# Optimization experiments

Hardware: AMD Instinct MI355X
Metric: run time of the kernel (lower is better)

The kernel has to match this reference:

```python
import jax, jax.numpy as jnp
import numpy as np

D_MODEL = 1024

def setup_inputs() -> dict:
    key = jax.random.key(0)
    ks = jax.random.split(key, 5)
    s = 1.0 / np.sqrt(D_MODEL)  # torch Linear default init scale-ish
    x = jax.random.normal(ks[0], (4, 2048, D_MODEL), dtype=jnp.float32)
    Wq = jax.random.normal(ks[1], (D_MODEL, D_MODEL), dtype=jnp.float32) * s
    Wk = jax.random.normal(ks[2], (D_MODEL, D_MODEL), dtype=jnp.float32) * s
    Wv = jax.random.normal(ks[3], (D_MODEL, D_MODEL), dtype=jnp.float32) * s
    Wo = jax.random.normal(ks[4], (D_MODEL, D_MODEL), dtype=jnp.float32) * s
    z = jnp.zeros((D_MODEL,), dtype=jnp.float32)
    return {"x": x, "Wq": Wq, "bq": z, "Wk": Wk, "bk": z, "Wv": Wv, "bv": z, "Wo": Wo, "bo": z}

def reference(x, Wq, bq, Wk, bk, Wv, bv, Wo, bo):
    # x: (B, S, D). Single-head causal attention, dropout in eval mode (identity).
    B, S, D = x.shape
    Q = jnp.einsum('bsd,ed->bse', x, Wq) + bq
    K = jnp.einsum('bsd,ed->bse', x, Wk) + bk
    V = jnp.einsum('bsd,ed->bse', x, Wv) + bv
    scores = jnp.einsum('bqd,bkd->bqk', Q, K) / jnp.sqrt(jnp.float32(D))
    causal = jnp.tril(jnp.ones((S, S), dtype=bool))  # (S, S)
    scores = jnp.where(causal, scores, -jnp.inf)
    weights = jax.nn.softmax(scores, axis=-1)
    attended = jnp.einsum('bqk,bkd->bqd', weights, V)
    out = jnp.einsum('bsd,ed->bse', attended, Wo) + bo
    return out
```

## Files before the change

### kernel.cpp

```cpp
#include <hip/hip_runtime.h>
#include <cstdint>
#include <cstddef>


#define D_MODEL 1024
#define SEQ     2048
#define BATCH   4

typedef unsigned short u16;
typedef __bf16 bf16_t;
typedef bf16_t bf16x8 __attribute__((ext_vector_type(8)));
typedef float  f32x4  __attribute__((ext_vector_type(4)));
typedef u16    u16x4  __attribute__((ext_vector_type(4)));

__device__ __forceinline__ u16 f2bf(float x) {
  union { float f; uint32_t u; } v; v.f = x;
  uint32_t r = v.u + 0x7fffu + ((v.u >> 16) & 1u);
  return (u16)(r >> 16);
}

__device__ __forceinline__ void gload_lds16(const u16* g, u16* l) {
  __builtin_amdgcn_global_load_lds((__attribute__((address_space(1))) void*)g,
                                   (__attribute__((address_space(3))) void*)l,
                                   16, 0, 0);
}

template <bool ROWSUM>
__device__ __forceinline__ void gemm_core(const u16* __restrict__ Ablk,
                                          const u16* __restrict__ Bblk,
                                          int lda, int ldb, int ksteps64,
                                          u16* As, u16* Bs,
                                          f32x4 acc[4][4], f32x4* rs) {
  const int tid  = threadIdx.x;
  const int wave = tid >> 6, lane = tid & 63;
  const int wr = (wave >> 1) * 64, wc = (wave & 1) * 64;
  const int frow = lane & 15, kq = lane >> 4;
  int sm[4], sk[4];
#pragma unroll
  for (int t = 0; t < 4; ++t) {
    const int ch = t * 256 + tid;
    sm[t] = ch >> 3;
    sk[t] = ((ch & 7) ^ (sm[t] & 7)) * 8;
  }
  int aoff[4], boff[4];
#pragma unroll
  for (int i = 0; i < 4; ++i) {
    const int ra = wr + i * 16 + frow;
    aoff[i] = ra * 64 + ((kq ^ (ra & 7)) * 8);
    const int rb = wc + i * 16 + frow;
    boff[i] = rb * 64 + ((kq ^ (rb & 7)) * 8);
  }
  bf16x8 ones;
  if (ROWSUM) {
#pragma unroll
    for (int r = 0; r < 8; ++r) ((u16*)&ones)[r] = 0x3F80;
  }

  for (int kt = 0; kt < ksteps64; ++kt) {
    __syncthreads();
    const int kb = kt * 64;
#pragma unroll
    for (int t = 0; t < 4; ++t)
      gload_lds16(Ablk + sm[t] * lda + kb + sk[t], As + (t * 256 + tid) * 8);
#pragma unroll
    for (int t = 0; t < 4; ++t)
      gload_lds16(Bblk + sm[t] * ldb + kb + sk[t], Bs + (t * 256 + tid) * 8);
    asm volatile("s_waitcnt vmcnt(0)" ::: "memory");
    __syncthreads();

#pragma unroll
    for (int kh = 0; kh < 2; ++kh) {
      const int xo = kh * 32;
      bf16x8 af[4], bf[4];
#pragma unroll
      for (int i = 0; i < 4; ++i) af[i] = *(const bf16x8*)(As + (aoff[i] ^ xo));
#pragma unroll
      for (int j = 0; j < 4; ++j) bf[j] = *(const bf16x8*)(Bs + (boff[j] ^ xo));
#pragma unroll
      for (int i = 0; i < 4; ++i)
#pragma unroll
        for (int j = 0; j < 4; ++j)
          acc[i][j] = __builtin_amdgcn_mfma_f32_16x16x32_bf16(af[i], bf[j], acc[i][j], 0, 0, 0);
      if (ROWSUM) {
#pragma unroll
        for (int i = 0; i < 4; ++i)
          rs[i] = __builtin_amdgcn_mfma_f32_16x16x32_bf16(af[i], ones, rs[i], 0, 0, 0);
      }
    }
  }
}

__global__ __launch_bounds__(256) void cvt_kernel(const float4* __restrict__ x,
                                                  const float4* __restrict__ wq,
                                                  const float4* __restrict__ wk,
                                                  const float4* __restrict__ wv,
                                                  const float4* __restrict__ wo,
                                                  u16* __restrict__ dst) {
  const int i = blockIdx.x * 256 + threadIdx.x;
  float4 v;
  if (i < 2097152) {
    v = x[i];
  } else {
    const int j = i - 2097152;
    const int w = j >> 18;
    const float4* s = (w == 0) ? wq : (w == 1) ? wk : (w == 2) ? wv : wo;
    v = s[j & 262143];
  }
  u16x4 o = {f2bf(v.x), f2bf(v.y), f2bf(v.z), f2bf(v.w)};
  *(u16x4*)(dst + (size_t)i * 4) = o;
}

__global__ void transposeW_kernel(const u16* __restrict__ src, u16* __restrict__ dst) {
  __shared__ u16 tile[32][33];
  const int r0 = blockIdx.x * 32, c0 = blockIdx.y * 32;
  const int tx = threadIdx.x, ty = threadIdx.y;
#pragma unroll
  for (int r = 0; r < 4; ++r)
    tile[ty + r * 8][tx] = src[(size_t)(r0 + ty + r * 8) * D_MODEL + c0 + tx];
  __syncthreads();
#pragma unroll
  for (int r = 0; r < 4; ++r)
    dst[(size_t)(c0 + ty + r * 8) * D_MODEL + r0 + tx] = tile[tx][ty + r * 8];
}

__global__ __launch_bounds__(256) void stageA_kernel(
    const u16* __restrict__ xb,
    const u16* __restrict__ WqB, const u16* __restrict__ WkB,
    const u16* __restrict__ WoB, const u16* __restrict__ WvT,
    const float* __restrict__ Wo32, const float* __restrict__ bv,
    const float* __restrict__ bq, const float* __restrict__ bk,
    u16* __restrict__ Qb, u16* __restrict__ Kb,
    u16* __restrict__ Wp, float* __restrict__ bp) {
  __shared__ __align__(16) u16 As[128 * 64];
  __shared__ __align__(16) u16 Bs[128 * 64];
  const int blk = blockIdx.x;
  const int lane = threadIdx.x & 63, wave = threadIdx.x >> 6;
  const int wr = (wave >> 1) * 64, wc = (wave & 1) * 64;
  const int cl = lane & 15, rl = (lane >> 4) * 4;

  if (blk < 64) {
    const int f0 = (blk >> 3) * 128, e0 = (blk & 7) * 128;
    f32x4 acc[4][4] = {};
    gemm_core<false>(WoB + (size_t)f0 * D_MODEL, WvT + (size_t)e0 * D_MODEL,
                     D_MODEL, D_MODEL, 16, As, Bs, acc, nullptr);
#pragma unroll
    for (int j = 0; j < 4; ++j) {
      const int col = e0 + wc + j * 16 + cl;
#pragma unroll
      for (int i = 0; i < 4; ++i)
#pragma unroll
        for (int r = 0; r < 4; ++r) {
          const int row = f0 + wr + i * 16 + rl + r;
          Wp[(size_t)row * D_MODEL + col] = f2bf(acc[i][j][r]);
        }
    }
  } else if (blk < 80) {
    const int f = (blk - 64) * 64 + (threadIdx.x >> 2);
    const int dq = threadIdx.x & 3;
    const float* row = Wo32 + (size_t)f * D_MODEL + dq * 256;
    const float* bvq = bv + dq * 256;
    float s = 0.f;
#pragma unroll 8
    for (int i = 0; i < 256; ++i) s += row[i] * bvq[i];
    s += __shfl_xor(s, 1);
    s += __shfl_xor(s, 2);
    if (dq == 0) bp[f] = s;
  } else {
    const int u = blk - 80;
    const int z = u >> 9;
    const u16*   W    = z ? WkB : WqB;
    const float* bias = z ? bk : bq;
    u16*         out  = z ? Kb : Qb;
    const int row0 = ((u >> 3) & 63) * 128, col0 = (u & 7) * 128;
    f32x4 acc[4][4] = {};
    gemm_core<false>(xb + (size_t)row0 * D_MODEL, W + (size_t)col0 * D_MODEL,
                     D_MODEL, D_MODEL, 16, As, Bs, acc, nullptr);
#pragma unroll
    for (int j = 0; j < 4; ++j) {
      const int col = col0 + wc + j * 16 + cl;
      const float bb = bias[col];
#pragma unroll
      for (int i = 0; i < 4; ++i)
#pragma unroll
        for (int r = 0; r < 4; ++r) {
          const int row = row0 + wr + i * 16 + rl + r;
          out[(size_t)row * D_MODEL + col] = f2bf(acc[i][j][r] + bb);
        }
    }
  }
}

__global__ __launch_bounds__(256) void stageB_kernel(
    const u16* __restrict__ xb, const u16* __restrict__ Wp,
    const float* __restrict__ bp,
    const u16* __restrict__ Qb, const u16* __restrict__ Kb,
    u16* __restrict__ Vt, u16* __restrict__ Eb) {
  __shared__ __align__(16) u16 As[128 * 64];
  __shared__ __align__(16) u16 Bs[128 * 64];
  const int blk = blockIdx.x;
  const int lane = threadIdx.x & 63, wave = threadIdx.x >> 6;
  const int wr = (wave >> 1) * 64, wc = (wave & 1) * 64;
  const int cl = lane & 15, rl = (lane >> 4) * 4;

  if (blk < 544) {
    const int b = blk / 136, t = blk % 136;
    int qi = (int)((sqrtf(8.0f * t + 1.0f) - 1.0f) * 0.5f);
    if ((qi + 1) * (qi + 2) / 2 <= t) ++qi;
    if (qi * (qi + 1) / 2 > t) --qi;
    const int ji = t - qi * (qi + 1) / 2;
    const u16* A  = Qb + (size_t)(b * SEQ + qi * 128) * D_MODEL;
    const u16* Bt = Kb + (size_t)(b * SEQ + ji * 128) * D_MODEL;
    f32x4 acc[4][4] = {};
    gemm_core<false>(A, Bt, D_MODEL, D_MODEL, 16, As, Bs, acc, nullptr);
    u16* out = Eb + (size_t)b * SEQ * SEQ;
#pragma unroll
    for (int i = 0; i < 4; ++i)
#pragma unroll
      for (int r = 0; r < 4; ++r) {
        const int q = qi * 128 + wr + i * 16 + rl + r;
#pragma unroll
        for (int j = 0; j < 4; ++j) {
          const int jj = ji * 128 + wc + j * 16 + cl;
          out[(size_t)q * SEQ + jj] =
              (jj <= q) ? f2bf(__expf(acc[i][j][r] * 0.03125f)) : (u16)0;
        }
      }
  } else {
    const int u = blk - 544;
    const int row0 = (u >> 3) * 128, col0 = (u & 7) * 128;
    f32x4 acc[4][4] = {};
    gemm_core<false>(xb + (size_t)row0 * D_MODEL, Wp + (size_t)col0 * D_MODEL,
                     D_MODEL, D_MODEL, 16, As, Bs, acc, nullptr);
    const int b = row0 >> 11;
    u16* vt = Vt + (size_t)b * D_MODEL * SEQ;
#pragma unroll
    for (int j = 0; j < 4; ++j) {
      const int col = col0 + wc + j * 16 + cl;
      const float bb = bp[col];
#pragma unroll
      for (int i = 0; i < 4; ++i) {
        const int s0 = (row0 & 2047) + wr + i * 16 + rl;
        u16x4 o = {f2bf(acc[i][j][0] + bb), f2bf(acc[i][j][1] + bb),
                   f2bf(acc[i][j][2] + bb), f2bf(acc[i][j][3] + bb)};
        *(u16x4*)(vt + (size_t)col * SEQ + s0) = o;
      }
    }
  }
}

__global__ __launch_bounds__(256) void pv_kernel(const u16* __restrict__ Eb,
                                                 const u16* __restrict__ Vt,
                                                 const float* __restrict__ bo,
                                                 float* __restrict__ Out) {
  __shared__ __align__(16) u16 As[128 * 64];
  __shared__ __align__(16) u16 Bs[128 * 64];
  const int qt = 15 - blockIdx.x, dt = blockIdx.y, b = blockIdx.z;
  const u16* A  = Eb + (size_t)b * SEQ * SEQ + (size_t)(qt * 128) * SEQ;
  const u16* Bt = Vt + (size_t)b * D_MODEL * SEQ + (size_t)(dt * 128) * SEQ;
  f32x4 acc[4][4] = {};
  f32x4 rs[4] = {};
  gemm_core<true>(A, Bt, SEQ, SEQ, (qt + 1) * 2, As, Bs, acc, rs);
  const int lane = threadIdx.x & 63, wave = threadIdx.x >> 6;
  const int wr = (wave >> 1) * 64, wc = (wave & 1) * 64;
  const int cl = lane & 15, rl = (lane >> 4) * 4;
#pragma unroll
  for (int i = 0; i < 4; ++i)
#pragma unroll
    for (int r = 0; r < 4; ++r) {
      const float invl = 1.0f / rs[i][r];
      const int row = b * SEQ + qt * 128 + wr + i * 16 + rl + r;
#pragma unroll
      for (int j = 0; j < 4; ++j) {
        const int col = dt * 128 + wc + j * 16 + cl;
        Out[(size_t)row * D_MODEL + col] = acc[i][j][r] * invl + bo[col];
      }
    }
}

extern "C" void kernel_launch(void* const* d_in, const int* in_sizes, int n_in,
                              void* d_out, int out_size, void* d_ws, size_t ws_size,
                              hipStream_t stream) {
  const float* x  = (const float*)d_in[0];
  const float* Wq = (const float*)d_in[1];
  const float* bq = (const float*)d_in[2];
  const float* Wk = (const float*)d_in[3];
  const float* bk = (const float*)d_in[4];
  const float* Wv = (const float*)d_in[5];
  const float* bv = (const float*)d_in[6];
  const float* Wo = (const float*)d_in[7];
  const float* bo = (const float*)d_in[8];
  float* out = (float*)d_out;
  char* ws = (char*)d_ws;

  u16*   xb  = (u16*)(ws);
  u16*   Wb  = (u16*)(ws + (16u << 20));
  u16*   Qb  = (u16*)(ws + (24u << 20));
  u16*   Kb  = (u16*)(ws + (40u << 20));
  u16*   Vt  = (u16*)(ws + (56u << 20));
  u16*   Eb  = (u16*)(ws + (72u << 20));
  u16*   WvT = (u16*)(ws + (104u << 20));
  u16*   Wp  = (u16*)(ws + (106u << 20));
  float* bp  = (float*)(ws + (108u << 20));

  cvt_kernel<<<12288, 256, 0, stream>>>((const float4*)x, (const float4*)Wq,
                                        (const float4*)Wk, (const float4*)Wv,
                                        (const float4*)Wo, xb);
  transposeW_kernel<<<dim3(32, 32), dim3(32, 8), 0, stream>>>(Wb + (2u << 20), WvT);
  stageA_kernel<<<1104, 256, 0, stream>>>(xb, Wb, Wb + (1u << 20), Wb + (3u << 20),
                                          WvT, Wo, bv, bq, bk, Qb, Kb, Wp, bp);
  stageB_kernel<<<1056, 256, 0, stream>>>(xb, Wp, bp, Qb, Kb, Vt, Eb);
  pv_kernel<<<dim3(16, 8, 4), 256, 0, stream>>>(Eb, Vt, bo, out);
}
```

Baseline: 287.0 us.

## Remap block indices so each XCD handles contiguous tile groups for L2 reuse

Rewrites the block-index-to-tile mapping in stageA QK projection, stageB scores and V projection, and the PV kernel so blocks that round-robin onto the same XCD (blk & 7) work on neighbouring row/column tiles. The goal is for tiles sharing A or B operands to land in the same XCD's L2, cutting redundant HBM traffic. The causal score tiles are split into off-diagonal 4x4 groups and diagonal triangles using lookup tables. This can unbalance per-XCD work, since diagonal groups and PV q-tiles differ in cost, and it relies on the hardware assigning workgroups round-robin across XCDs.

```diff
diff --git a/kernel.cpp b/kernel.cpp
--- a/kernel.cpp
+++ b/kernel.cpp
@@ -166,12 +166,15 @@
     s += __shfl_xor(s, 2);
     if (dq == 0) bp[f] = s;
   } else {
-    const int u = blk - 80;
-    const int z = u >> 9;
+    const int v = blk - 80;
+    const int c = v & 7, s = v >> 3;
+    const int row0 = (c * 8 + (s >> 4)) * 128;
+    const int cz = s & 15;
+    const int z = cz >> 3;
+    const int col0 = (cz & 7) * 128;
     const u16*   W    = z ? WkB : WqB;
     const float* bias = z ? bk : bq;
     u16*         out  = z ? Kb : Qb;
-    const int row0 = ((u >> 3) & 63) * 128, col0 = (u & 7) * 128;
     f32x4 acc[4][4] = {};
     gemm_core<false>(xb + (size_t)row0 * D_MODEL, W + (size_t)col0 * D_MODEL,
                      D_MODEL, D_MODEL, 16, As, Bs, acc, nullptr);
@@ -203,11 +206,28 @@
   const int cl = lane & 15, rl = (lane >> 4) * 4;
 
   if (blk < 544) {
-    const int b = blk / 136, t = blk % 136;
-    int qi = (int)((sqrtf(8.0f * t + 1.0f) - 1.0f) * 0.5f);
-    if ((qi + 1) * (qi + 2) / 2 <= t) ++qi;
-    if (qi * (qi + 1) / 2 > t) --qi;
-    const int ji = t - qi * (qi + 1) / 2;
+    const int c = blk & 7, s = blk >> 3;
+    int b, qi, ji;
+    if (s < 48) {
+      static const int sq_tab[6] = {1, 2, 2, 3, 3, 3};
+      static const int sj_tab[6] = {0, 0, 1, 0, 1, 2};
+      const int fi = c * 3 + (s >> 4);
+      const int off = s & 15;
+      b = fi / 6;
+      const int fs = fi % 6;
+      qi = sq_tab[fs] * 4 + (off >> 2);
+      ji = sj_tab[fs] * 4 + (off & 3);
+    } else {
+      static const int di_tab[10] = {0, 1, 1, 2, 2, 2, 3, 3, 3, 3};
+      static const int dj_tab[10] = {0, 0, 1, 0, 1, 2, 0, 1, 2, 3};
+      const int k = (s - 48) / 10;
+      const int off = (s - 48) % 10;
+      const int di = c * 2 + k;
+      b = di >> 2;
+      const int dk = di & 3;
+      qi = dk * 4 + di_tab[off];
+      ji = dk * 4 + dj_tab[off];
+    }
     const u16* A  = Qb + (size_t)(b * SEQ + qi * 128) * D_MODEL;
     const u16* Bt = Kb + (size_t)(b * SEQ + ji * 128) * D_MODEL;
     f32x4 acc[4][4] = {};
@@ -226,8 +246,10 @@
         }
       }
   } else {
-    const int u = blk - 544;
-    const int row0 = (u >> 3) * 128, col0 = (u & 7) * 128;
+    const int v = blk - 544;
+    const int c = v & 7, s = v >> 3;
+    const int row0 = (c * 8 + (s >> 3)) * 128;
+    const int col0 = (s & 7) * 128;
     f32x4 acc[4][4] = {};
     gemm_core<false>(xb + (size_t)row0 * D_MODEL, Wp + (size_t)col0 * D_MODEL,
                      D_MODEL, D_MODEL, 16, As, Bs, acc, nullptr);
@@ -254,7 +276,11 @@
                                                  float* __restrict__ Out) {
   __shared__ __align__(16) u16 As[128 * 64];
   __shared__ __align__(16) u16 Bs[128 * 64];
-  const int qt = 15 - blockIdx.x, dt = blockIdx.y, b = blockIdx.z;
+  const int u = blockIdx.x;
+  const int c = u & 7, s = u >> 3;
+  const int b  = c >> 1;
+  const int dt = (c & 1) * 4 + (s >> 4);
+  const int qt = 15 - (s & 15);
   const u16* A  = Eb + (size_t)b * SEQ * SEQ + (size_t)(qt * 128) * SEQ;
   const u16* Bt = Vt + (size_t)b * D_MODEL * SEQ + (size_t)(dt * 128) * SEQ;
   f32x4 acc[4][4] = {};
@@ -309,5 +335,5 @@
   stageA_kernel<<<1104, 256, 0, stream>>>(xb, Wb, Wb + (1u << 20), Wb + (3u << 20),
                                           WvT, Wo, bv, bq, bk, Qb, Kb, Wp, bp);
   stageB_kernel<<<1056, 256, 0, stream>>>(xb, Wp, bp, Qb, Kb, Vt, Eb);
-  pv_kernel<<<dim3(16, 8, 4), 256, 0, stream>>>(Eb, Vt, bo, out);
-}
+  pv_kernel<<<512, 256, 0, stream>>>(Eb, Vt, bo, out);
+}
```

Measured after the change: 268.2 us. 1.07x faster.
